# Optimization experiments

Hardware: AMD Instinct MI355X
Metric: run time of the kernel (lower is better)

The kernel has to match this reference:

```python
import jax, jax.numpy as jnp
import numpy as np

N_NODES = 100000
N_EDGES = 1600000
DIM_IN = 64
DIM_OUT = 40
K_HOPS = 3


def setup_inputs() -> dict:
    key = jax.random.key(0)
    ks = jax.random.split(key, 6)
    x = jax.random.normal(ks[0], (N_NODES, DIM_IN), dtype=jnp.float32)
    edge_index = jax.random.randint(ks[1], (2, N_EDGES), 0, N_NODES, dtype=jnp.int64)
    W_sgc = jax.random.normal(ks[2], (DIM_IN, DIM_IN), dtype=jnp.float32) * (1.0 / np.sqrt(DIM_IN))
    b_sgc = jax.random.normal(ks[3], (DIM_IN,), dtype=jnp.float32) * 0.02
    W_head = jax.random.normal(ks[4], (DIM_IN, DIM_OUT), dtype=jnp.float32) * (1.0 / np.sqrt(DIM_IN))
    b_head = jax.random.normal(ks[5], (DIM_OUT,), dtype=jnp.float32) * 0.02
    return {"x": x, "edge_index": edge_index, "W_sgc": W_sgc, "b_sgc": b_sgc,
            "W_head": W_head, "b_head": b_head}


def _sgc_forward(x, src, dst, norm, W_sgc, b_sgc, W_head, b_head):
    n = x.shape[0]
    # K-hop normalized adjacency propagation: x <- A_hat @ x, K times
    for _ in range(K_HOPS):
        x = jax.ops.segment_sum(norm[:, None] * x[src], dst, num_segments=n)
    # SGConv linear projection
    x = x @ W_sgc + b_sgc
    # dropout is identity at inference (training=False)
    # post-MP node head: Linear(dim_in -> dim_out)
    return x @ W_head + b_head


def reference(x, edge_index, W_sgc, b_sgc, W_head, b_head):
    n = x.shape[0]
    # gcn_norm with self-loops (PyG SGConv default):
    loop = jnp.arange(n, dtype=edge_index.dtype)
    src = jnp.concatenate([edge_index[0], loop])  # message source j
    dst = jnp.concatenate([edge_index[1], loop])  # message target i
    ew = jnp.ones(src.shape[0], dtype=x.dtype)
    deg = jax.ops.segment_sum(ew, dst, num_segments=n)
    dinv = jnp.where(deg > 0, jax.lax.rsqrt(deg), 0.0)
    norm = dinv[src] * dinv[dst]  # [E + N]
    return _sgc_forward(x, src, dst, norm, W_sgc, b_sgc, W_head, b_head)
```

## Files before the change

kernel.cpp:

```cpp
#include <hip/hip_runtime.h>
#include <hip/hip_bf16.h>
#include <hip/hip_fp16.h>

#define DIMI 64
#define DIMO 40

#define NBK_SHIFT 9
#define NPBK 512
#define NBKMAX 256
#define BCAP 9216
#define CHUNK 4096


__global__ void k_zero(int* __restrict__ p, int n) {
    int i = blockIdx.x * blockDim.x + threadIdx.x;
    if (i < n) p[i] = 0;
}

__global__ void k_binA(const int* __restrict__ src, const int* __restrict__ dst,
                       int* __restrict__ bcnt, int* __restrict__ ebP,
                       int E, int nbk) {
    __shared__ int h[NBKMAX];
    __shared__ int lb[NBKMAX];
    __shared__ int lc[NBKMAX];
    __shared__ int gb[NBKMAX];
    __shared__ int eb[CHUNK];
    __shared__ unsigned char ebB[CHUNK];
    int t = threadIdx.x;
    int e0 = blockIdx.x * CHUNK;
    int e1 = min(e0 + CHUNK, E);
    int nE = e1 - e0;
    h[t] = 0;
    __syncthreads();
    int d[CHUNK / 256], s[CHUNK / 256];
    #pragma unroll
    for (int u = 0; u < CHUNK / 256; u++) {
        int idx = e0 + t + u * 256;
        if (idx < e1) {
            d[u] = dst[idx];
            s[u] = src[idx];
            atomicAdd(&h[d[u] >> NBK_SHIFT], 1);
        }
    }
    __syncthreads();
    int orig = h[t];
    for (int o = 1; o < 256; o <<= 1) {
        int v = (t >= o) ? h[t - o] : 0;
        __syncthreads();
        h[t] += v;
        __syncthreads();
    }
    lb[t] = h[t] - orig;
    lc[t] = 0;
    gb[t] = orig ? atomicAdd(&bcnt[t], orig) : 0;
    __syncthreads();
    #pragma unroll
    for (int u = 0; u < CHUNK / 256; u++) {
        int idx = e0 + t + u * 256;
        if (idx < e1) {
            int b = d[u] >> NBK_SHIFT;
            int r = atomicAdd(&lc[b], 1);
            int slot = lb[b] + r;
            eb[slot] = (s[u] << NBK_SHIFT) | (d[u] & (NPBK - 1));
            ebB[slot] = (unsigned char)b;
        }
    }
    __syncthreads();
    for (int i = t; i < nE; i += 256) {
        int b = ebB[i];
        int slot = gb[b] + (i - lb[b]);
        if (slot < BCAP) ebP[(size_t)b * BCAP + slot] = eb[i];
    }
}

__global__ void k_scan_bcnt(const int* __restrict__ bcnt, int* __restrict__ bbase, int nbk) {
    __shared__ int s[256];
    int t = threadIdx.x;
    int orig = (t < nbk) ? min(bcnt[t], BCAP) : 0;
    s[t] = orig;
    __syncthreads();
    for (int o = 1; o < 256; o <<= 1) {
        int v = (t >= o) ? s[t - o] : 0;
        __syncthreads();
        s[t] += v;
        __syncthreads();
    }
    if (t < nbk) bbase[t] = s[t] - orig;
}

__global__ void k_binBC(const int* __restrict__ bcnt, const int* __restrict__ bbase,
                        const int* __restrict__ ebP,
                        int* __restrict__ off, float* __restrict__ dinv,
                        int* __restrict__ col, int N) {
    __shared__ int sh[NPBK];
    __shared__ int so[NPBK];
    __shared__ int slc[NPBK];
    __shared__ int scol[BCAP];
    int b = blockIdx.x, t = threadIdx.x;
    sh[t] = 0; sh[t + 256] = 0;
    __syncthreads();
    int n = min(bcnt[b], BCAP);
    size_t base = (size_t)b * BCAP;
    for (int i = t; i < n; i += 256)
        atomicAdd(&sh[ebP[base + i] & (NPBK - 1)], 1);
    __syncthreads();
    so[t] = sh[t]; so[t + 256] = sh[t + 256];
    __syncthreads();
    for (int o = 1; o < NPBK; o <<= 1) {
        int v0 = (t >= o) ? sh[t - o] : 0;
        int v1 = (t + 256 >= o) ? sh[t + 256 - o] : 0;
        __syncthreads();
        sh[t] += v0; sh[t + 256] += v1;
        __syncthreads();
    }
    int gbase = bbase[b];
    int d0 = b << NBK_SHIFT;
    #pragma unroll
    for (int half = 0; half < 2; half++) {
        int j = t + half * 256;
        int orig = so[j];
        int excl = sh[j] - orig;
        int dd = d0 + j;
        if (dd < N) {
            off[dd] = gbase + excl;
            dinv[dd] = rsqrtf((float)(orig + 1));
        }
        so[j] = excl;
        slc[j] = 0;
    }
    if (t == 0 && b == (int)gridDim.x - 1) off[N] = gbase + n;
    __syncthreads();
    for (int i = t; i < n; i += 256) {
        int e = ebP[base + i];
        int local = e & (NPBK - 1);
        int r = atomicAdd(&slc[local], 1);
        scol[so[local] + r] = e >> NBK_SHIFT;
    }
    __syncthreads();
    for (int i = t; i < n; i += 256) col[gbase + i] = scol[i];
}


__global__ void k_hist(const int* __restrict__ dst, int* __restrict__ counts, int E) {
    int i = blockIdx.x * blockDim.x + threadIdx.x;
    if (i < E) atomicAdd(&counts[dst[i]], 1);
}

__global__ void k_scatter(const int* __restrict__ src, const int* __restrict__ dst,
                          const int* __restrict__ off, int* __restrict__ cursor,
                          int* __restrict__ col, int E) {
    int i = blockIdx.x * blockDim.x + threadIdx.x;
    if (i < E) {
        int d = dst[i];
        int p = off[d] + atomicAdd(&cursor[d], 1);
        col[p] = src[i];
    }
}

__global__ void k_block_sums(const int* __restrict__ counts, int* __restrict__ partial, int n) {
    __shared__ int s[256];
    int i = blockIdx.x * 256 + threadIdx.x;
    s[threadIdx.x] = (i < n) ? counts[i] : 0;
    __syncthreads();
    for (int st = 128; st > 0; st >>= 1) {
        if (threadIdx.x < st) s[threadIdx.x] += s[threadIdx.x + st];
        __syncthreads();
    }
    if (threadIdx.x == 0) partial[blockIdx.x] = s[0];
}

__global__ void k_scan_partials(int* partial, int nb) {
    __shared__ int s[1024];
    int t = threadIdx.x;
    int orig = (t < nb) ? partial[t] : 0;
    s[t] = orig;
    __syncthreads();
    for (int o = 1; o < 1024; o <<= 1) {
        int v = (t >= o) ? s[t - o] : 0;
        __syncthreads();
        s[t] += v;
        __syncthreads();
    }
    if (t < nb) partial[t] = s[t] - orig;
}

__global__ void k_scan_final(const int* __restrict__ counts, const int* __restrict__ partial,
                             int* __restrict__ off, float* __restrict__ dinv, int n) {
    __shared__ int s[256];
    int t = threadIdx.x;
    int i = blockIdx.x * 256 + t;
    int orig = (i < n) ? counts[i] : 0;
    s[t] = orig;
    __syncthreads();
    for (int o = 1; o < 256; o <<= 1) {
        int v = (t >= o) ? s[t - o] : 0;
        __syncthreads();
        s[t] += v;
        __syncthreads();
    }
    if (i < n) {
        off[i] = s[t] - orig + partial[blockIdx.x];
        dinv[i] = rsqrtf((float)(orig + 1));
        if (i == n - 1) off[n] = s[t] + partial[blockIdx.x];
    }
}


__global__ void k_wc(const float* __restrict__ Wsgc, const float* __restrict__ bsgc,
                     const float* __restrict__ Whead, const float* __restrict__ bhead,
                     float* __restrict__ Wc, float* __restrict__ bc) {
    __shared__ float sA[DIMI * DIMI];
    __shared__ float sB[DIMI * DIMO];
    int t = threadIdx.x;
    for (int i = t; i < DIMI * DIMI; i += 256) sA[i] = Wsgc[i];
    for (int i = t; i < DIMI * DIMO; i += 256) sB[i] = Whead[i];
    __syncthreads();
    for (int o = t; o < DIMI * DIMO; o += 256) {
        int k = o / DIMO, j = o % DIMO;
        float a = 0.f;
        #pragma unroll
        for (int m = 0; m < DIMI; m++) a += sA[k * DIMI + m] * sB[m * DIMO + j];
        Wc[o] = a;
    }
    if (t < DIMO) {
        float a = bhead[t];
        #pragma unroll
        for (int m = 0; m < DIMI; m++) a += bsgc[m] * sB[m * DIMO + t];
        bc[t] = a;
    }
}

__global__ void k_projU(const float* __restrict__ x, const float* __restrict__ Wc,
                        const float* __restrict__ dinv, __half* __restrict__ y, int N) {
    __shared__ float sW[DIMI * DIMO];
    int t = threadIdx.x;
    for (int i = t; i < DIMI * DIMO; i += 256) sW[i] = Wc[i];
    __syncthreads();
    int node = blockIdx.x * 256 + t;
    if (node >= N) return;
    float di = dinv[node];
    const float4* xr = (const float4*)(x + (size_t)node * DIMI);
    float acc[DIMO];
    #pragma unroll
    for (int j = 0; j < DIMO; j++) acc[j] = 0.f;
    for (int k4 = 0; k4 < DIMI / 4; k4++) {
        float4 xv = xr[k4];
        int k = k4 * 4;
        #pragma unroll
        for (int j = 0; j < DIMO; j++)
            acc[j] += xv.x * sW[k * DIMO + j] + xv.y * sW[(k + 1) * DIMO + j]
                    + xv.z * sW[(k + 2) * DIMO + j] + xv.w * sW[(k + 3) * DIMO + j];
    }
    __half2* y2 = (__half2*)(y + (size_t)node * DIMO);
    #pragma unroll
    for (int p = 0; p < DIMO / 2; p++)
        y2[p] = __floats2half2_rn(di * acc[2 * p], di * acc[2 * p + 1]);
}

__global__ void k_hop(const __half* __restrict__ xin, __half* __restrict__ xout,
                      float* __restrict__ outF,
                      const int* __restrict__ off, const float* __restrict__ dinv,
                      const int* __restrict__ col, const float* __restrict__ bc,
                      int finalHop, int N) {
    int gtid = blockIdx.x * blockDim.x + threadIdx.x;
    int node = gtid >> 6;
    int lane = threadIdx.x & 63;
    if (node >= N) return;
    int l = lane < DIMO ? lane : DIMO - 1;
    int rs = off[node];
    int cnt = off[node + 1] - rs;
    int cidx = (lane < cnt) ? col[rs + lane] : node;
    float acc = __half2float(xin[(size_t)node * DIMO + l]);
    int cmain = cnt < 64 ? cnt : 64;
    int e = 0;
    for (; e + 16 <= cmain; e += 16) {
        float v[16];
        #pragma unroll
        for (int u = 0; u < 16; u++) {
            int c = __shfl(cidx, e + u, 64);
            v[u] = __half2float(xin[(size_t)c * DIMO + l]);
        }
        float s01 = (v[0] + v[1]) + (v[2] + v[3]);
        float s23 = (v[4] + v[5]) + (v[6] + v[7]);
        float s45 = (v[8] + v[9]) + (v[10] + v[11]);
        float s67 = (v[12] + v[13]) + (v[14] + v[15]);
        acc += (s01 + s23) + (s45 + s67);
    }
    for (; e + 4 <= cmain; e += 4) {
        float v[4];
        #pragma unroll
        for (int u = 0; u < 4; u++) {
            int c = __shfl(cidx, e + u, 64);
            v[u] = __half2float(xin[(size_t)c * DIMO + l]);
        }
        acc += (v[0] + v[1]) + (v[2] + v[3]);
    }
    for (; e < cmain; e++) {
        int c = __shfl(cidx, e, 64);
        acc += __half2float(xin[(size_t)c * DIMO + l]);
    }
    for (int e2 = 64; e2 < cnt; e2++)
        acc += __half2float(xin[(size_t)col[rs + e2] * DIMO + l]);
    float di = dinv[node];
    if (lane < DIMO) {
        if (finalHop) outF[(size_t)node * DIMO + lane] = di * acc + bc[lane];
        else          xout[(size_t)node * DIMO + lane] = __float2half(di * di * acc);
    }
}


extern "C" void kernel_launch(void* const* d_in, const int* in_sizes, int n_in,
                              void* d_out, int out_size, void* d_ws, size_t ws_size,
                              hipStream_t stream) {
    const float* x     = (const float*)d_in[0];
    const int*   ei    = (const int*)d_in[1];
    const float* Wsgc  = (const float*)d_in[2];
    const float* bsgc  = (const float*)d_in[3];
    const float* Whead = (const float*)d_in[4];
    const float* bhead = (const float*)d_in[5];
    float* out = (float*)d_out;

    const int N = in_sizes[0] / DIMI;
    const int E = in_sizes[1] / 2;
    const int* src = ei;
    const int* dst = ei + E;
    const int nbk = (N + NPBK - 1) >> NBK_SHIFT;

    char* w = (char*)d_ws;
    auto carve = [&](size_t bytes) {
        char* p = w;
        w += (bytes + 255) & ~(size_t)255;
        return p;
    };
    int*   counts  = (int*)  carve((size_t)N * 4);
    int*   cursor  = (int*)  carve((size_t)N * 4);
    int*   off     = (int*)  carve((size_t)(N + 1) * 4);
    float* dinv    = (float*)carve((size_t)N * 4);
    int*   partial = (int*)  carve(1024 * 4);
    int*   col     = (int*)  carve((size_t)E * 4);
    float* Wc      = (float*)carve(DIMI * DIMO * 4);
    float* bc      = (float*)carve(DIMO * 4);
    int*   bcnt    = (int*)  carve((size_t)nbk * 4);
    int*   bbase   = (int*)  carve((size_t)nbk * 4);
    size_t xbytes  = (size_t)N * DIMO * 2;
    size_t ebytes  = (size_t)nbk * BCAP * 4;
    size_t ubytes  = ebytes > 2 * xbytes ? ebytes : 2 * xbytes;
    char*  uni     = carve(ubytes);
    int*    ebP = (int*)uni;
    __half* xA  = (__half*)uni;
    __half* xB  = (__half*)(uni + xbytes);
    size_t total_need = (size_t)(w - (char*)d_ws);
    const bool useBuckets = (ws_size >= total_need) && (nbk <= NBKMAX);

    const int B = 256;
    int nbN = (N + B - 1) / B;
    int nbE = (E + B - 1) / B;

    k_wc<<<1, 256, 0, stream>>>(Wsgc, bsgc, Whead, bhead, Wc, bc);

    if (useBuckets) {
        k_zero<<<(nbk + B - 1) / B, B, 0, stream>>>(bcnt, nbk);
        int nbA = (E + CHUNK - 1) / CHUNK;
        k_binA<<<nbA, B, 0, stream>>>(src, dst, bcnt, ebP, E, nbk);
        k_scan_bcnt<<<1, 256, 0, stream>>>(bcnt, bbase, nbk);
        k_binBC<<<nbk, B, 0, stream>>>(bcnt, bbase, ebP, off, dinv, col, N);
    } else {
        k_zero<<<nbN, B, 0, stream>>>(counts, N);
        k_zero<<<nbN, B, 0, stream>>>(cursor, N);
        k_hist<<<nbE, B, 0, stream>>>(dst, counts, E);
        k_block_sums<<<nbN, B, 0, stream>>>(counts, partial, N);
        k_scan_partials<<<1, 1024, 0, stream>>>(partial, nbN);
        k_scan_final<<<nbN, B, 0, stream>>>(counts, partial, off, dinv, N);
        k_scatter<<<nbE, B, 0, stream>>>(src, dst, off, cursor, col, E);
    }

    k_projU<<<nbN, B, 0, stream>>>(x, Wc, dinv, xA, N);

    int hopBlocks = (N * 64 + B - 1) / B;
    k_hop<<<hopBlocks, B, 0, stream>>>(xA, xB, out, off, dinv, col, bc, 0, N);
    k_hop<<<hopBlocks, B, 0, stream>>>(xB, xA, out, off, dinv, col, bc, 0, N);
    k_hop<<<hopBlocks, B, 0, stream>>>(xA, xB, out, off, dinv, col, bc, 1, N);
}
```

Baseline: 218.9 us.

## Split each hop into two passes over source-node halves for cache locality

```diff
diff --git a/kernel.cpp b/kernel.cpp
--- a/kernel.cpp
+++ b/kernel.cpp
@@ -73,68 +73,76 @@
     }
 }
 
-__global__ void k_scan_bcnt(const int* __restrict__ bcnt, int* __restrict__ bbase, int nbk) {
-    __shared__ int s[256];
-    int t = threadIdx.x;
-    int orig = (t < nbk) ? min(bcnt[t], BCAP) : 0;
-    s[t] = orig;
-    __syncthreads();
-    for (int o = 1; o < 256; o <<= 1) {
-        int v = (t >= o) ? s[t - o] : 0;
-        __syncthreads();
-        s[t] += v;
-        __syncthreads();
-    }
-    if (t < nbk) bbase[t] = s[t] - orig;
-}
-
-__global__ void k_binBC(const int* __restrict__ bcnt, const int* __restrict__ bbase,
-                        const int* __restrict__ ebP,
-                        int* __restrict__ off, float* __restrict__ dinv,
-                        int* __restrict__ col, int N) {
-    __shared__ int sh[NPBK];
-    __shared__ int so[NPBK];
-    __shared__ int slc[NPBK];
+__global__ void k_binBC(const int* __restrict__ bcnt, const int* __restrict__ ebP,
+                        int* __restrict__ off, int* __restrict__ mid,
+                        float* __restrict__ dinv, int* __restrict__ col,
+                        int N, int nbk, int nHalf) {
+    __shared__ int sb[256];
+    __shared__ int sh[1024];
+    __shared__ int ssum[256];
+    __shared__ int so[1024];
+    __shared__ int slc[1024];
     __shared__ int scol[BCAP];
     int b = blockIdx.x, t = threadIdx.x;
-    sh[t] = 0; sh[t + 256] = 0;
-    __syncthreads();
+    int v = (t < nbk) ? min(bcnt[t], BCAP) : 0;
+    sb[t] = v;
+    __syncthreads();
+    for (int o = 1; o < 256; o <<= 1) {
+        int u = (t >= o) ? sb[t - o] : 0;
+        __syncthreads();
+        sb[t] += u;
+        __syncthreads();
+    }
+    int gbase = (b > 0) ? sb[b - 1] : 0;
     int n = min(bcnt[b], BCAP);
+    sh[t] = 0; sh[t + 256] = 0; sh[t + 512] = 0; sh[t + 768] = 0;
+    __syncthreads();
     size_t base = (size_t)b * BCAP;
-    for (int i = t; i < n; i += 256)
-        atomicAdd(&sh[ebP[base + i] & (NPBK - 1)], 1);
-    __syncthreads();
-    so[t] = sh[t]; so[t + 256] = sh[t + 256];
-    __syncthreads();
-    for (int o = 1; o < NPBK; o <<= 1) {
-        int v0 = (t >= o) ? sh[t - o] : 0;
-        int v1 = (t + 256 >= o) ? sh[t + 256 - o] : 0;
-        __syncthreads();
-        sh[t] += v0; sh[t + 256] += v1;
-        __syncthreads();
-    }
-    int gbase = bbase[b];
-    int d0 = b << NBK_SHIFT;
-    #pragma unroll
-    for (int half = 0; half < 2; half++) {
-        int j = t + half * 256;
-        int orig = so[j];
-        int excl = sh[j] - orig;
-        int dd = d0 + j;
-        if (dd < N) {
-            off[dd] = gbase + excl;
-            dinv[dd] = rsqrtf((float)(orig + 1));
-        }
-        so[j] = excl;
-        slc[j] = 0;
-    }
-    if (t == 0 && b == (int)gridDim.x - 1) off[N] = gbase + n;
-    __syncthreads();
     for (int i = t; i < n; i += 256) {
         int e = ebP[base + i];
-        int local = e & (NPBK - 1);
-        int r = atomicAdd(&slc[local], 1);
-        scol[so[local] + r] = e >> NBK_SHIFT;
+        int key = ((e & (NPBK - 1)) << 1) | ((e >> NBK_SHIFT) >= nHalf ? 1 : 0);
+        atomicAdd(&sh[key], 1);
+    }
+    __syncthreads();
+    int c0 = sh[4 * t], c1 = sh[4 * t + 1], c2 = sh[4 * t + 2], c3 = sh[4 * t + 3];
+    int tsum = c0 + c1 + c2 + c3;
+    ssum[t] = tsum;
+    __syncthreads();
+    for (int o = 1; o < 256; o <<= 1) {
+        int u = (t >= o) ? ssum[t - o] : 0;
+        __syncthreads();
+        ssum[t] += u;
+        __syncthreads();
+    }
+    int eb0 = ssum[t] - tsum;
+    so[4 * t] = eb0;
+    so[4 * t + 1] = eb0 + c0;
+    so[4 * t + 2] = eb0 + c0 + c1;
+    so[4 * t + 3] = eb0 + c0 + c1 + c2;
+    slc[4 * t] = 0; slc[4 * t + 1] = 0; slc[4 * t + 2] = 0; slc[4 * t + 3] = 0;
+    int d0 = b << NBK_SHIFT;
+    {
+        int dd = d0 + 2 * t;
+        if (dd < N) {
+            off[dd] = gbase + eb0;
+            mid[dd] = gbase + eb0 + c0;
+            dinv[dd] = rsqrtf((float)(c0 + c1 + 1));
+        }
+        dd = d0 + 2 * t + 1;
+        if (dd < N) {
+            off[dd] = gbase + eb0 + c0 + c1;
+            mid[dd] = gbase + eb0 + c0 + c1 + c2;
+            dinv[dd] = rsqrtf((float)(c2 + c3 + 1));
+        }
+    }
+    if (t == 0 && b == nbk - 1) off[N] = gbase + n;
+    __syncthreads();
+    for (int i = t; i < n; i += 256) {
+        int e = ebP[base + i];
+        int srcv = e >> NBK_SHIFT;
+        int key = ((e & (NPBK - 1)) << 1) | (srcv >= nHalf ? 1 : 0);
+        int r = atomicAdd(&slc[key], 1);
+        scol[so[key] + r] = srcv;
     }
     __syncthreads();
     for (int i = t; i < n; i += 256) col[gbase + i] = scol[i];
@@ -185,7 +193,8 @@
 }
 
 __global__ void k_scan_final(const int* __restrict__ counts, const int* __restrict__ partial,
-                             int* __restrict__ off, float* __restrict__ dinv, int n) {
+                             int* __restrict__ off, int* __restrict__ mid,
+                             float* __restrict__ dinv, int n) {
     __shared__ int s[256];
     int t = threadIdx.x;
     int i = blockIdx.x * 256 + t;
@@ -200,6 +209,7 @@
     }
     if (i < n) {
         off[i] = s[t] - orig + partial[blockIdx.x];
+        mid[i] = s[t] + partial[blockIdx.x];
         dinv[i] = rsqrtf((float)(orig + 1));
         if (i == n - 1) off[n] = s[t] + partial[blockIdx.x];
     }
@@ -208,10 +218,12 @@
 
 __global__ void k_wc(const float* __restrict__ Wsgc, const float* __restrict__ bsgc,
                      const float* __restrict__ Whead, const float* __restrict__ bhead,
-                     float* __restrict__ Wc, float* __restrict__ bc) {
+                     float* __restrict__ Wc, float* __restrict__ bc,
+                     int* __restrict__ bcnt, int nbk) {
     __shared__ float sA[DIMI * DIMI];
     __shared__ float sB[DIMI * DIMO];
     int t = threadIdx.x;
+    for (int i = t; i < nbk; i += 256) bcnt[i] = 0;
     for (int i = t; i < DIMI * DIMI; i += 256) sA[i] = Wsgc[i];
     for (int i = t; i < DIMI * DIMO; i += 256) sB[i] = Whead[i];
     __syncthreads();
@@ -257,34 +269,71 @@
         y2[p] = __floats2half2_rn(di * acc[2 * p], di * acc[2 * p + 1]);
 }
 
-__global__ void k_hop(const __half* __restrict__ xin, __half* __restrict__ xout,
-                      float* __restrict__ outF,
-                      const int* __restrict__ off, const float* __restrict__ dinv,
-                      const int* __restrict__ col, const float* __restrict__ bc,
-                      int finalHop, int N) {
+__global__ void k_hopA(const __half* __restrict__ xin, __half* __restrict__ xpart,
+                       const int* __restrict__ off, const int* __restrict__ mid,
+                       const int* __restrict__ col, int N) {
     int gtid = blockIdx.x * blockDim.x + threadIdx.x;
     int node = gtid >> 6;
     int lane = threadIdx.x & 63;
     if (node >= N) return;
     int l = lane < DIMO ? lane : DIMO - 1;
     int rs = off[node];
-    int cnt = off[node + 1] - rs;
+    int cnt = mid[node] - rs;
     int cidx = (lane < cnt) ? col[rs + lane] : node;
     float acc = __half2float(xin[(size_t)node * DIMO + l]);
     int cmain = cnt < 64 ? cnt : 64;
     int e = 0;
-    for (; e + 16 <= cmain; e += 16) {
-        float v[16];
-        #pragma unroll
-        for (int u = 0; u < 16; u++) {
+    for (; e + 8 <= cmain; e += 8) {
+        float v[8];
+        #pragma unroll
+        for (int u = 0; u < 8; u++) {
             int c = __shfl(cidx, e + u, 64);
             v[u] = __half2float(xin[(size_t)c * DIMO + l]);
         }
-        float s01 = (v[0] + v[1]) + (v[2] + v[3]);
-        float s23 = (v[4] + v[5]) + (v[6] + v[7]);
-        float s45 = (v[8] + v[9]) + (v[10] + v[11]);
-        float s67 = (v[12] + v[13]) + (v[14] + v[15]);
-        acc += (s01 + s23) + (s45 + s67);
+        acc += ((v[0] + v[1]) + (v[2] + v[3])) + ((v[4] + v[5]) + (v[6] + v[7]));
+    }
+    for (; e + 4 <= cmain; e += 4) {
+        float v[4];
+        #pragma unroll
+        for (int u = 0; u < 4; u++) {
+            int c = __shfl(cidx, e + u, 64);
+            v[u] = __half2float(xin[(size_t)c * DIMO + l]);
+        }
+        acc += (v[0] + v[1]) + (v[2] + v[3]);
+    }
+    for (; e < cmain; e++) {
+        int c = __shfl(cidx, e, 64);
+        acc += __half2float(xin[(size_t)c * DIMO + l]);
+    }
+    for (int e2 = 64; e2 < cnt; e2++)
+        acc += __half2float(xin[(size_t)col[rs + e2] * DIMO + l]);
+    if (lane < DIMO) xpart[(size_t)node * DIMO + lane] = __float2half(acc);
+}
+
+__global__ void k_hopB(const __half* __restrict__ xin, __half* __restrict__ xpart,
+                       float* __restrict__ outF,
+                       const int* __restrict__ off, const int* __restrict__ mid,
+                       const int* __restrict__ col, const float* __restrict__ dinv,
+                       const float* __restrict__ bc, int finalHop, int N) {
+    int gtid = blockIdx.x * blockDim.x + threadIdx.x;
+    int node = gtid >> 6;
+    int lane = threadIdx.x & 63;
+    if (node >= N) return;
+    int l = lane < DIMO ? lane : DIMO - 1;
+    int rs = mid[node];
+    int cnt = off[node + 1] - rs;
+    int cidx = (lane < cnt) ? col[rs + lane] : node;
+    float acc = __half2float(xpart[(size_t)node * DIMO + l]);
+    int cmain = cnt < 64 ? cnt : 64;
+    int e = 0;
+    for (; e + 8 <= cmain; e += 8) {
+        float v[8];
+        #pragma unroll
+        for (int u = 0; u < 8; u++) {
+            int c = __shfl(cidx, e + u, 64);
+            v[u] = __half2float(xin[(size_t)c * DIMO + l]);
+        }
+        acc += ((v[0] + v[1]) + (v[2] + v[3])) + ((v[4] + v[5]) + (v[6] + v[7]));
     }
     for (; e + 4 <= cmain; e += 4) {
         float v[4];
@@ -304,7 +353,7 @@
     float di = dinv[node];
     if (lane < DIMO) {
         if (finalHop) outF[(size_t)node * DIMO + lane] = di * acc + bc[lane];
-        else          xout[(size_t)node * DIMO + lane] = __float2half(di * di * acc);
+        else          xpart[(size_t)node * DIMO + lane] = __float2half(di * di * acc);
     }
 }
 
@@ -325,6 +374,7 @@
     const int* src = ei;
     const int* dst = ei + E;
     const int nbk = (N + NPBK - 1) >> NBK_SHIFT;
+    const int nHalf = N / 2;
 
     char* w = (char*)d_ws;
     auto carve = [&](size_t bytes) {
@@ -335,13 +385,13 @@
     int*   counts  = (int*)  carve((size_t)N * 4);
     int*   cursor  = (int*)  carve((size_t)N * 4);
     int*   off     = (int*)  carve((size_t)(N + 1) * 4);
+    int*   mid     = (int*)  carve((size_t)N * 4);
     float* dinv    = (float*)carve((size_t)N * 4);
     int*   partial = (int*)  carve(1024 * 4);
     int*   col     = (int*)  carve((size_t)E * 4);
     float* Wc      = (float*)carve(DIMI * DIMO * 4);
     float* bc      = (float*)carve(DIMO * 4);
     int*   bcnt    = (int*)  carve((size_t)nbk * 4);
-    int*   bbase   = (int*)  carve((size_t)nbk * 4);
     size_t xbytes  = (size_t)N * DIMO * 2;
     size_t ebytes  = (size_t)nbk * BCAP * 4;
     size_t ubytes  = ebytes > 2 * xbytes ? ebytes : 2 * xbytes;
@@ -356,28 +406,29 @@
     int nbN = (N + B - 1) / B;
     int nbE = (E + B - 1) / B;
 
-    k_wc<<<1, 256, 0, stream>>>(Wsgc, bsgc, Whead, bhead, Wc, bc);
+    k_wc<<<1, 256, 0, stream>>>(Wsgc, bsgc, Whead, bhead, Wc, bc, bcnt, nbk);
 
     if (useBuckets) {
-        k_zero<<<(nbk + B - 1) / B, B, 0, stream>>>(bcnt, nbk);
         int nbA = (E + CHUNK - 1) / CHUNK;
         k_binA<<<nbA, B, 0, stream>>>(src, dst, bcnt, ebP, E, nbk);
-        k_scan_bcnt<<<1, 256, 0, stream>>>(bcnt, bbase, nbk);
-        k_binBC<<<nbk, B, 0, stream>>>(bcnt, bbase, ebP, off, dinv, col, N);
+        k_binBC<<<nbk, B, 0, stream>>>(bcnt, ebP, off, mid, dinv, col, N, nbk, nHalf);
     } else {
         k_zero<<<nbN, B, 0, stream>>>(counts, N);
         k_zero<<<nbN, B, 0, stream>>>(cursor, N);
         k_hist<<<nbE, B, 0, stream>>>(dst, counts, E);
         k_block_sums<<<nbN, B, 0, stream>>>(counts, partial, N);
         k_scan_partials<<<1, 1024, 0, stream>>>(partial, nbN);
-        k_scan_final<<<nbN, B, 0, stream>>>(counts, partial, off, dinv, N);
+        k_scan_final<<<nbN, B, 0, stream>>>(counts, partial, off, mid, dinv, N);
         k_scatter<<<nbE, B, 0, stream>>>(src, dst, off, cursor, col, E);
     }
 
     k_projU<<<nbN, B, 0, stream>>>(x, Wc, dinv, xA, N);
 
     int hopBlocks = (N * 64 + B - 1) / B;
-    k_hop<<<hopBlocks, B, 0, stream>>>(xA, xB, out, off, dinv, col, bc, 0, N);
-    k_hop<<<hopBlocks, B, 0, stream>>>(xB, xA, out, off, dinv, col, bc, 0, N);
-    k_hop<<<hopBlocks, B, 0, stream>>>(xA, xB, out, off, dinv, col, bc, 1, N);
-}
+    k_hopA<<<hopBlocks, B, 0, stream>>>(xA, xB, off, mid, col, N);
+    k_hopB<<<hopBlocks, B, 0, stream>>>(xA, xB, out, off, mid, col, dinv, bc, 0, N);
+    k_hopA<<<hopBlocks, B, 0, stream>>>(xB, xA, off, mid, col, N);
+    k_hopB<<<hopBlocks, B, 0, stream>>>(xB, xA, out, off, mid, col, dinv, bc, 0, N);
+    k_hopA<<<hopBlocks, B, 0, stream>>>(xA, xB, off, mid, col, N);
+    k_hopB<<<hopBlocks, B, 0, stream>>>(xA, xB, out, off, mid, col, dinv, bc, 1, N);
+}
```

Result: slower. 277.2 us (+26.6%).
